# Kernel tuning notes

Measured on AMD Instinct MI355X. Metric: run time of the kernel, lower is better.

The kernel has to match this reference:

```python
import jax, jax.numpy as jnp
import numpy as np

B, N, M, DIM, H, DH = 2, 2048, 2048, 512, 8, 64
INNER = H * DH
SCALE = DH ** -0.5  # cosine_sim=False default
EPS = 1e-5


def layer_norm(x, g, b):
    mu = x.mean(-1, keepdims=True)
    var = ((x - mu) ** 2).mean(-1, keepdims=True)
    return (x - mu) * jax.lax.rsqrt(var + EPS) * g + b


def setup_inputs() -> dict:
    key = jax.random.key(0)
    ks = jax.random.split(key, 8)
    x = jax.random.normal(ks[0], (B, N, DIM), dtype=jnp.float32)
    context = jax.random.normal(ks[1], (B, M, DIM), dtype=jnp.float32)
    mask = jax.random.randint(ks[2], (B, M), 0, 2).astype(bool)
    Wq = jax.random.normal(ks[3], (DIM, INNER), dtype=jnp.float32) * 0.02
    Wkv = jax.random.normal(ks[4], (DIM, 2 * INNER), dtype=jnp.float32) * 0.02
    Wo = jax.random.normal(ks[5], (INNER, DIM), dtype=jnp.float32) * 0.02
    ln_g = jnp.ones((DIM,), jnp.float32)
    ln_b = jnp.zeros((DIM,), jnp.float32)
    lno_g = jnp.ones((DIM,), jnp.float32)
    lno_b = jnp.zeros((DIM,), jnp.float32)
    return {"x": x, "context": context, "mask": mask, "ln_g": ln_g, "ln_b": ln_b,
            "Wq": Wq, "Wkv": Wkv, "Wo": Wo, "lno_g": lno_g, "lno_b": lno_b}


def reference(x, context, mask, ln_g, ln_b, Wq, Wkv, Wo, lno_g, lno_b):
    b, n, _ = x.shape
    xn = layer_norm(x, ln_g, ln_b)
    ctx = context  # norm_context=False -> Identity
    q = (xn @ Wq).reshape(b, n, H, DH).transpose(0, 2, 1, 3)          # b h n d
    kv = ctx @ Wkv
    k, v = jnp.split(kv, 2, axis=-1)
    k = k.reshape(b, -1, H, DH).transpose(0, 2, 1, 3)                 # b h m d
    v = v.reshape(b, -1, H, DH).transpose(0, 2, 1, 3)
    q = q * SCALE
    k = k * SCALE
    sim = jnp.einsum('bhid,bhjd->bhij', q, k)                         # b h n m (256 MB)
    max_neg = -jnp.finfo(sim.dtype).max
    sim = jnp.where(mask[:, None, None, :], sim, max_neg)
    attn = jax.nn.softmax(sim.astype(jnp.float32), axis=-1).astype(sim.dtype)
    out = jnp.einsum('bhij,bhjd->bhid', attn, v)
    out = out.transpose(0, 2, 1, 3).reshape(b, n, INNER)
    return layer_norm(out @ Wo, lno_g, lno_b)
```

## Files before the change

kernel.cpp:

```cpp
#include <hip/hip_runtime.h>
#include <stdint.h>

typedef float f32x4 __attribute__((ext_vector_type(4)));
typedef float f32x16 __attribute__((ext_vector_type(16)));
typedef __bf16 bf16x8 __attribute__((ext_vector_type(8)));
typedef unsigned int uint2v __attribute__((ext_vector_type(2)));

#define MFMA16(a,b,c) __builtin_amdgcn_mfma_f32_16x16x32_bf16((a),(b),(c),0,0,0)
#define MFMA32(a,b,c) __builtin_amdgcn_mfma_f32_32x32x16_bf16((a),(b),(c),0,0,0)

__device__ __forceinline__ unsigned short f2bf(float f){
  unsigned int u = __float_as_uint(f);
  u += 0x7FFFu + ((u >> 16) & 1u);
  return (unsigned short)(u >> 16);
}

__device__ __forceinline__ unsigned cvtpk(float lo, float hi){
  unsigned r;
  asm volatile("v_cvt_pk_bf16_f32 %0, %1, %2" : "=v"(r) : "v"(lo), "v"(hi));
  return r;
}

__device__ __forceinline__ float fexp2(float x){
#if __has_builtin(__builtin_amdgcn_exp2f)
  return __builtin_amdgcn_exp2f(x);
#else
  return exp2f(x);
#endif
}

__device__ __forceinline__ void plswap(unsigned &a, unsigned &b){
#if __has_builtin(__builtin_amdgcn_permlane32_swap)
  uint2v r = __builtin_amdgcn_permlane32_swap(a, b, false, false);
  a = r[0]; b = r[1];
#else
  unsigned xa = __shfl_xor(a, 32), xb = __shfl_xor(b, 32);
  int hi = (threadIdx.x & 63) >> 5;
  unsigned na = hi ? xb : a;
  unsigned nb = hi ? b : xa;
  a = na; b = nb;
#endif
}

__device__ __forceinline__ void stage16(const unsigned short* g, unsigned short* l){
  __builtin_amdgcn_global_load_lds(
      (const __attribute__((address_space(1))) void*)g,
      (__attribute__((address_space(3))) void*)l, 16, 0, 0);
}

__global__ __launch_bounds__(256) void k_prep(
    const float* __restrict__ Wq, const float* __restrict__ Wkv, const float* __restrict__ Wo,
    const float* __restrict__ x, const float* __restrict__ ln_g, const float* __restrict__ ln_b,
    const float* __restrict__ ctx, const int* __restrict__ mask,
    unsigned short* __restrict__ WqT, unsigned short* __restrict__ WkvT, unsigned short* __restrict__ WoT,
    unsigned short* __restrict__ xn, unsigned short* __restrict__ cb, unsigned int* __restrict__ mb)
{
  __shared__ float tile[32][33];
  const int bid = blockIdx.x, t = threadIdx.x;
  if (bid < 1024) {
    const float* W; unsigned short* WT; int N, bx, by;
    if (bid < 256)      { W = Wq;  WT = WqT;  N = 512;  bx = bid & 15;        by = bid >> 4; }
    else if (bid < 768) { W = Wkv; WT = WkvT; N = 1024; bx = (bid-256) & 31;  by = (bid-256) >> 5; }
    else                { W = Wo;  WT = WoT;  N = 512;  bx = (bid-768) & 15;  by = (bid-768) >> 4; }
    const int tx = t & 31, ty = t >> 5;
    #pragma unroll
    for (int i = 0; i < 4; i++)
      tile[ty + i*8][tx] = W[(size_t)(by*32 + ty + i*8) * N + bx*32 + tx];
    __syncthreads();
    #pragma unroll
    for (int i = 0; i < 4; i++)
      WT[(size_t)(bx*32 + ty + i*8) * 512 + by*32 + tx] = f2bf(tile[tx][ty + i*8]);
  } else if (bid < 2048) {
    int row = (bid - 1024) * 4 + (t >> 6);
    int lane = t & 63;
    const float4* xr = (const float4*)(x + (size_t)row * 512);
    float4 a = xr[lane], c = xr[64 + lane];
    float s = a.x + a.y + a.z + a.w + c.x + c.y + c.z + c.w;
    #pragma unroll
    for (int o = 32; o; o >>= 1) s += __shfl_xor(s, o);
    float mu = s * (1.0f / 512.0f);
    float va = (a.x-mu)*(a.x-mu) + (a.y-mu)*(a.y-mu) + (a.z-mu)*(a.z-mu) + (a.w-mu)*(a.w-mu)
             + (c.x-mu)*(c.x-mu) + (c.y-mu)*(c.y-mu) + (c.z-mu)*(c.z-mu) + (c.w-mu)*(c.w-mu);
    #pragma unroll
    for (int o = 32; o; o >>= 1) va += __shfl_xor(va, o);
    float inv = rsqrtf(va * (1.0f / 512.0f) + 1e-5f);
    const float4* gp = (const float4*)ln_g;
    const float4* bp = (const float4*)ln_b;
    float4 g0 = gp[lane], g1 = gp[64 + lane], b0 = bp[lane], b1 = bp[64 + lane];
    ushort4* op = (ushort4*)(xn + (size_t)row * 512);
    op[lane]      = make_ushort4(f2bf((a.x-mu)*inv*g0.x + b0.x), f2bf((a.y-mu)*inv*g0.y + b0.y),
                                 f2bf((a.z-mu)*inv*g0.z + b0.z), f2bf((a.w-mu)*inv*g0.w + b0.w));
    op[64 + lane] = make_ushort4(f2bf((c.x-mu)*inv*g1.x + b1.x), f2bf((c.y-mu)*inv*g1.y + b1.y),
                                 f2bf((c.z-mu)*inv*g1.z + b1.z), f2bf((c.w-mu)*inv*g1.w + b1.w));
  } else if (bid < 4096) {
    int i = (bid - 2048) * 256 + t;
    float4 v = ((const float4*)ctx)[i];
    ((ushort4*)cb)[i] = make_ushort4(f2bf(v.x), f2bf(v.y), f2bf(v.z), f2bf(v.w));
  } else {
    int g = (bid - 4096) * 4 + (t >> 6);
    int ln = t & 63;
    int v = mask[g * 64 + ln];
    unsigned long long bb = __ballot(v != 0);
    if (ln == 0) { mb[g*2] = (unsigned)bb; mb[g*2+1] = (unsigned)(bb >> 32); }
  }
}

__global__ __launch_bounds__(256) void k_layernorm_f(
    const float* __restrict__ X, const float* __restrict__ G,
    const float* __restrict__ Bt, float* __restrict__ out)
{
  int row = blockIdx.x * 4 + (threadIdx.x >> 6);
  int lane = threadIdx.x & 63;
  const float4* xr = (const float4*)(X + (size_t)row * 512);
  float4 a = xr[lane], c = xr[64 + lane];
  float s = a.x + a.y + a.z + a.w + c.x + c.y + c.z + c.w;
  #pragma unroll
  for (int o = 32; o; o >>= 1) s += __shfl_xor(s, o);
  float mu = s * (1.0f / 512.0f);
  float va = (a.x-mu)*(a.x-mu) + (a.y-mu)*(a.y-mu) + (a.z-mu)*(a.z-mu) + (a.w-mu)*(a.w-mu)
           + (c.x-mu)*(c.x-mu) + (c.y-mu)*(c.y-mu) + (c.z-mu)*(c.z-mu) + (c.w-mu)*(c.w-mu);
  #pragma unroll
  for (int o = 32; o; o >>= 1) va += __shfl_xor(va, o);
  float inv = rsqrtf(va * (1.0f / 512.0f) + 1e-5f);
  const float4* gp = (const float4*)G;
  const float4* bp = (const float4*)Bt;
  float4 g0 = gp[lane], g1 = gp[64 + lane], b0 = bp[lane], b1 = bp[64 + lane];
  float4 y0, y1;
  y0.x = (a.x-mu)*inv*g0.x + b0.x; y0.y = (a.y-mu)*inv*g0.y + b0.y;
  y0.z = (a.z-mu)*inv*g0.z + b0.z; y0.w = (a.w-mu)*inv*g0.w + b0.w;
  y1.x = (c.x-mu)*inv*g1.x + b1.x; y1.y = (c.y-mu)*inv*g1.y + b1.y;
  y1.z = (c.z-mu)*inv*g1.z + b1.z; y1.w = (c.w-mu)*inv*g1.w + b1.w;
  float4* op = (float4*)(out + (size_t)row * 512);
  op[lane] = y0; op[64 + lane] = y1;
}

template<int MODE>
__device__ __forceinline__ void gemm_body(
    const unsigned short* __restrict__ A, const unsigned short* __restrict__ BT,
    void* __restrict__ out0, void* __restrict__ out1, int bx, int by,
    unsigned short* smem)
{
  unsigned short* As = smem;
  unsigned short* Bs = smem + 2*64*64;
  const int t = threadIdx.x;
  const int lane = t & 63, l16 = lane & 15, lhi = lane >> 4;
  const int w = t >> 6, wm = w >> 1, wn = w & 1;
  const int rowBase = by * 64;
  const int colBase = bx * 128;
  const int srr = lane >> 3, scw = lane & 7;

  f32x4 acc[2][4];
  #pragma unroll
  for (int i = 0; i < 2; i++)
    #pragma unroll
    for (int j = 0; j < 4; j++)
      acc[i][j] = f32x4{0.f, 0.f, 0.f, 0.f};

  auto STAGE = [&](int buf, int kt) {
    unsigned short* Ab = As + buf * 4096;
    unsigned short* Bb = Bs + buf * 8192;
    #pragma unroll
    for (int i = 0; i < 2; i++) {
      int rr = i * 32 + w * 8 + srr;
      stage16(A + (size_t)(rowBase + rr) * 512 + kt * 64 + ((scw ^ (rr & 7)) * 8),
              Ab + (i * 32 + w * 8) * 64);
    }
    #pragma unroll
    for (int i = 0; i < 4; i++) {
      int rr = i * 32 + w * 8 + srr;
      stage16(BT + (size_t)(colBase + rr) * 512 + kt * 64 + ((scw ^ (rr & 7)) * 8),
              Bb + (i * 32 + w * 8) * 64);
    }
  };

  STAGE(0, 0);
  __syncthreads();
  for (int kt = 0; kt < 8; ++kt) {
    const int buf = kt & 1;
    if (kt < 7) STAGE(buf ^ 1, kt + 1);
    const char* Ab = (const char*)(As + buf * 4096);
    const char* Bb = (const char*)(Bs + buf * 8192);
    #pragma unroll
    for (int ks = 0; ks < 2; ++ks) {
      bf16x8 af[2], bb[4];
      #pragma unroll
      for (int mi = 0; mi < 2; mi++) {
        int rr = wm * 32 + mi * 16 + l16;
        int cc = ks * 4 + lhi;
        af[mi] = *(const bf16x8*)(Ab + rr * 128 + ((cc ^ (rr & 7)) * 16));
      }
      #pragma unroll
      for (int ni = 0; ni < 4; ni++) {
        int rr = wn * 64 + ni * 16 + l16;
        int cc = ks * 4 + lhi;
        bb[ni] = *(const bf16x8*)(Bb + rr * 128 + ((cc ^ (rr & 7)) * 16));
      }
      #pragma unroll
      for (int mi = 0; mi < 2; mi++)
        #pragma unroll
        for (int ni = 0; ni < 4; ni++)
          acc[mi][ni] = MFMA16(af[mi], bb[ni], acc[mi][ni]);
    }
    __syncthreads();
  }

  if constexpr (MODE == 2) {
    const int r0 = rowBase + wm * 32 + lhi * 4;
    const int c0 = colBase + wn * 64 + l16;
    #pragma unroll
    for (int mi = 0; mi < 2; mi++)
      #pragma unroll
      for (int ni = 0; ni < 4; ni++)
        #pragma unroll
        for (int r = 0; r < 4; r++)
          ((float*)out0)[(size_t)(r0 + mi * 16 + r) * 512 + c0 + ni * 16] = acc[mi][ni][r];
  } else {
    unsigned short* stg = smem;
    const bool isV = (MODE == 1) && (colBase >= 512);
    if (!isV) {
      #pragma unroll
      for (int mi = 0; mi < 2; mi++) {
        int rl = wm * 32 + mi * 16 + lhi * 4;
        int tl = rl >> 5;
        #pragma unroll
        for (int ni = 0; ni < 4; ni++) {
          int cl = wn * 64 + ni * 16 + l16;
          int hl = cl >> 6, d = cl & 63;
          int rbase = (hl * 2 + tl) * 2048 + (d >> 4) * 512 + 256 * ((d >> 3) & 1) + (d & 7);
          #pragma unroll
          for (int r = 0; r < 4; r++)
            stg[rbase + ((rl + r) & 31) * 8] = f2bf(acc[mi][ni][r]);
        }
      }
    } else {
      #pragma unroll
      for (int mi = 0; mi < 2; mi++) {
        int rl = wm * 32 + mi * 16 + lhi * 4;
        int tl = rl >> 5, kvr = rl & 31;
        #pragma unroll
        for (int ni = 0; ni < 4; ni++) {
          int cl = wn * 64 + ni * 16 + l16;
          int hl = cl >> 6, d = cl & 63;
          int off = (hl * 2 + tl) * 2048 + (d >> 5) * 1024 + ((kvr >> 4) & 1) * 512
                  + ((d & 31) + 32 * ((kvr >> 3) & 1)) * 8 + (kvr & 7);
          ushort4 p = make_ushort4(f2bf(acc[mi][ni][0]), f2bf(acc[mi][ni][1]),
                                   f2bf(acc[mi][ni][2]), f2bf(acc[mi][ni][3]));
          *(ushort4*)(stg + off) = p;
        }
      }
    }
    __syncthreads();
    const int bb2 = rowBase >> 11;
    const int hh0 = (colBase & 511) >> 6;
    const int tile0 = (rowBase & 2047) >> 5;
    unsigned short* gout = (unsigned short*)(isV ? out1 : out0);
    #pragma unroll
    for (int ridx = 0; ridx < 4; ridx++) {
      int hl = ridx >> 1, tl = ridx & 1;
      size_t gb = ((size_t)((bb2 * 8 + hh0 + hl) * 64 + tile0 + tl)) * 2048 + t * 8;
      *(uint4*)(gout + gb) = *(const uint4*)(stg + ridx * 2048 + t * 8);
    }
  }
}

__global__ __launch_bounds__(256, 2) void k_qkv(
    const unsigned short* __restrict__ xn, const unsigned short* __restrict__ WqT,
    unsigned short* __restrict__ Qp,
    const unsigned short* __restrict__ cb, const unsigned short* __restrict__ WkvT,
    unsigned short* __restrict__ Kp, unsigned short* __restrict__ Vp)
{
  __shared__ __align__(16) unsigned short smem[2*64*64 + 2*128*64];
  const int bid = blockIdx.x;
  const int xcd = bid & 7, loc = bid >> 3;
  const int mloc = loc / 12, ct = loc % 12;
  const int mtile = xcd * 8 + mloc;
  if (ct < 4) gemm_body<0>(xn, WqT, Qp, nullptr, ct, mtile, smem);
  else        gemm_body<1>(cb, WkvT, Kp, Vp, ct - 4, mtile, smem);
}

__global__ __launch_bounds__(256, 2) void k_oproj(
    const unsigned short* __restrict__ ao, const unsigned short* __restrict__ WoT,
    float* __restrict__ proj)
{
  __shared__ __align__(16) unsigned short smem[2*64*64 + 2*128*64];
  const int bid = blockIdx.x;
  const int xcd = bid & 7, loc = bid >> 3;
  const int mloc = loc >> 2, ct = loc & 3;
  const int mtile = xcd * 8 + mloc;
  gemm_body<2>(ao, WoT, proj, nullptr, ct, mtile, smem);
}

__global__ __launch_bounds__(256, 3) void k_attn(
    const unsigned short* __restrict__ Qp, const unsigned short* __restrict__ Kp,
    const unsigned short* __restrict__ Vp, const unsigned int* __restrict__ mb,
    unsigned short* __restrict__ O)
{
  __shared__ __align__(16) float mbuf[3][64][34];
  const int t = threadIdx.x, lane = t & 63, q5 = lane & 31, hi = lane >> 5;
  const int w = t >> 6;
  const int bid = blockIdx.x;
  const int bh = (bid & 7) * 2 + (bid >> 9);
  const int qt = (bid >> 3) & 63;
  const int q0 = qt * 32;
  const int b = bh >> 3, h = bh & 7;
  const float C2f = 0.022542110013890053f;

  bf16x8 qf[4];
  {
    const unsigned short* qp = Qp + (size_t)(bh * 64 + qt) * 2048 + lane * 8;
    #pragma unroll
    for (int kk = 0; kk < 4; kk++) qf[kk] = *(const bf16x8*)(qp + kk * 512);
  }
  const unsigned short* kpb = Kp + (size_t)bh * 131072 + lane * 8;
  const unsigned short* vpb = Vp + (size_t)bh * 131072 + lane * 8;
  const unsigned int* mbp = mb + b * 64;

  float mrun = -3e38f, lrun = 0.f;
  f32x16 acc0, acc1;
  #pragma unroll
  for (int i = 0; i < 16; i++) { acc0[i] = 0.f; acc1[i] = 0.f; }

  bf16x8 kf[4], vf[4];
  auto loadK = [&](int tile) {
    #pragma unroll
    for (int kk = 0; kk < 4; kk++)
      kf[kk] = *(const bf16x8*)(kpb + (size_t)tile * 2048 + kk * 512);
  };
  auto loadV = [&](int tile) {
    #pragma unroll
    for (int i = 0; i < 4; i++)
      vf[i] = *(const bf16x8*)(vpb + (size_t)tile * 2048 + i * 512);
  };

  const int tb = w * 16;
  loadK(tb); loadV(tb);
  for (int it = 0; it < 16; ++it) {
    const int ti = tb + it;

    f32x16 s;
    #pragma unroll
    for (int i = 0; i < 16; i++) s[i] = 0.f;
    #pragma unroll
    for (int kk = 0; kk < 4; kk++) s = MFMA32(kf[kk], qf[kk], s);
    if (it < 15) loadK(ti + 1);

    float m0 = fmaxf(fmaxf(s[0], s[1]),  fmaxf(s[2], s[3]));
    float m1 = fmaxf(fmaxf(s[4], s[5]),  fmaxf(s[6], s[7]));
    float m2 = fmaxf(fmaxf(s[8], s[9]),  fmaxf(s[10], s[11]));
    float m3 = fmaxf(fmaxf(s[12], s[13]), fmaxf(s[14], s[15]));
    float tmax = fmaxf(fmaxf(m0, m1), fmaxf(m2, m3));
    tmax = fmaxf(tmax, __shfl_xor(tmax, 32));
    if (!__all(tmax <= mrun + 400.f)) {
      float mnew = fmaxf(mrun, tmax);
      float sf = fexp2((mrun - mnew) * C2f);
      lrun *= sf;
      #pragma unroll
      for (int i = 0; i < 16; i++) { acc0[i] *= sf; acc1[i] *= sf; }
      mrun = mnew;
    }
    unsigned mh = mbp[ti] >> (hi * 4);
    float nb = -mrun * C2f;
    float p[16];
    #pragma unroll
    for (int r = 0; r < 16; r++) {
      float pv = fexp2(fmaf(s[r], C2f, nb));
      p[r] = ((mh >> ((r & 3) + 8 * (r >> 2))) & 1u) ? pv : 0.f;
    }
    float rsa = (p[0] + p[1]) + (p[2] + p[3]);
    float rsb = (p[4] + p[5]) + (p[6] + p[7]);
    float rsc = (p[8] + p[9]) + (p[10] + p[11]);
    float rsd = (p[12] + p[13]) + (p[14] + p[15]);
    float rs = (rsa + rsb) + (rsc + rsd);
    rs += __shfl_xor(rs, 32);
    lrun += rs;

    unsigned wd[8];
    #pragma unroll
    for (int i = 0; i < 8; i++) wd[i] = cvtpk(p[2 * i], p[2 * i + 1]);
    plswap(wd[0], wd[2]); plswap(wd[1], wd[3]);
    plswap(wd[4], wd[6]); plswap(wd[5], wd[7]);
    union { unsigned u[4]; bf16x8 v; } U0, U1;
    U0.u[0] = wd[0]; U0.u[1] = wd[1]; U0.u[2] = wd[2]; U0.u[3] = wd[3];
    U1.u[0] = wd[4]; U1.u[1] = wd[5]; U1.u[2] = wd[6]; U1.u[3] = wd[7];

    acc0 = MFMA32(vf[0], U0.v, acc0);
    acc0 = MFMA32(vf[1], U1.v, acc0);
    acc1 = MFMA32(vf[2], U0.v, acc1);
    acc1 = MFMA32(vf[3], U1.v, acc1);
    if (it < 15) loadV(ti + 1);
  }

  if (w) {
    #pragma unroll
    for (int i = 0; i < 16; i++) { mbuf[w-1][lane][i] = acc0[i]; mbuf[w-1][lane][16 + i] = acc1[i]; }
    mbuf[w-1][lane][32] = mrun; mbuf[w-1][lane][33] = lrun;
  }
  __syncthreads();
  if (!w) {
    float mo[3], lo[3];
    #pragma unroll
    for (int wv = 0; wv < 3; wv++) { mo[wv] = mbuf[wv][lane][32]; lo[wv] = mbuf[wv][lane][33]; }
    float mN = fmaxf(fmaxf(mrun, mo[0]), fmaxf(mo[1], mo[2]));
    float sf0 = fexp2((mrun - mN) * C2f);
    float sfv[3];
    float lsum = lrun * sf0;
    #pragma unroll
    for (int wv = 0; wv < 3; wv++) { sfv[wv] = fexp2((mo[wv] - mN) * C2f); lsum += lo[wv] * sfv[wv]; }
    float linv = 1.f / lsum;
    float a2[32];
    #pragma unroll
    for (int i = 0; i < 16; i++) {
      float v0 = acc0[i] * sf0, v1 = acc1[i] * sf0;
      #pragma unroll
      for (int wv = 0; wv < 3; wv++) {
        v0 += mbuf[wv][lane][i] * sfv[wv];
        v1 += mbuf[wv][lane][16 + i] * sfv[wv];
      }
      a2[i] = v0 * linv;
      a2[16 + i] = v1 * linv;
    }
    unsigned short* ot = (unsigned short*)&mbuf[0][0][0];
    #pragma unroll
    for (int d2 = 0; d2 < 2; d2++)
      #pragma unroll
      for (int i = 0; i < 8; i++) {
        int d0 = ((2 * i) & 3) + 8 * (i >> 1) + 4 * hi + 32 * d2;
        unsigned wv2 = cvtpk(a2[d2 * 16 + 2 * i], a2[d2 * 16 + 2 * i + 1]);
        *(unsigned*)(ot + q5 * 72 + d0) = wv2;
      }
    #pragma unroll
    for (int it2 = 0; it2 < 4; ++it2) {
      int row = (lane >> 3) + it2 * 8, ch = lane & 7;
      uint4 val = *(const uint4*)(ot + row * 72 + ch * 8);
      *(uint4*)(O + ((size_t)(b * 2048 + q0 + row)) * 512 + h * 64 + ch * 8) = val;
    }
  }
}

extern "C" void kernel_launch(void* const* d_in, const int* in_sizes, int n_in,
                              void* d_out, int out_size, void* d_ws, size_t ws_size,
                              hipStream_t stream) {
  const float* x     = (const float*)d_in[0];
  const float* ctx   = (const float*)d_in[1];
  const int*   mask  = (const int*)d_in[2];
  const float* ln_g  = (const float*)d_in[3];
  const float* ln_b  = (const float*)d_in[4];
  const float* Wq    = (const float*)d_in[5];
  const float* Wkv   = (const float*)d_in[6];
  const float* Wo    = (const float*)d_in[7];
  const float* lno_g = (const float*)d_in[8];
  const float* lno_b = (const float*)d_in[9];
  float* out = (float*)d_out;

  char* ws = (char*)d_ws;
  unsigned short* WqT  = (unsigned short*)(ws + 0);
  unsigned short* WkvT = (unsigned short*)(ws + (size_t)1 * (1 << 19));
  unsigned short* WoT  = (unsigned short*)(ws + (size_t)3 * (1 << 19));
  unsigned short* xn   = (unsigned short*)(ws + (size_t)2  * (1 << 20));
  unsigned short* cb   = (unsigned short*)(ws + (size_t)6  * (1 << 20));
  unsigned short* Qp   = (unsigned short*)(ws + (size_t)10 * (1 << 20));
  unsigned short* Kp   = (unsigned short*)(ws + (size_t)14 * (1 << 20));
  unsigned short* Vp   = (unsigned short*)(ws + (size_t)18 * (1 << 20));
  unsigned short* ao   = (unsigned short*)(ws + (size_t)22 * (1 << 20));
  float* proj          = (float*)(ws + (size_t)26 * (1 << 20));
  unsigned int* mbw    = (unsigned int*)(ws + (size_t)26 * (1 << 20));

  k_prep<<<4112, 256, 0, stream>>>(Wq, Wkv, Wo, x, ln_g, ln_b, ctx, mask,
                                   WqT, WkvT, WoT, xn, cb, mbw);
  k_qkv<<<768, 256, 0, stream>>>(xn, WqT, Qp, cb, WkvT, Kp, Vp);
  k_attn<<<1024, 256, 0, stream>>>(Qp, Kp, Vp, mbw, ao);
  k_oproj<<<256, 256, 0, stream>>>(ao, WoT, proj);
  k_layernorm_f<<<1024, 256, 0, stream>>>(proj, lno_g, lno_b, out);
}
```

Measured before the change: 63.13 us.

## Give each attention wave its own query tile over all keys, dropping split-K merge

Measured after the change: 78.68 us. 1.25x slower.

```diff
diff --git a/kernel.cpp b/kernel.cpp
--- a/kernel.cpp
+++ b/kernel.cpp
@@ -290,17 +290,17 @@
   gemm_body<2>(ao, WoT, proj, nullptr, ct, mtile, smem);
 }
 
-__global__ __launch_bounds__(256, 3) void k_attn(
+__global__ __launch_bounds__(256, 2) void k_attn(
     const unsigned short* __restrict__ Qp, const unsigned short* __restrict__ Kp,
     const unsigned short* __restrict__ Vp, const unsigned int* __restrict__ mb,
     unsigned short* __restrict__ O)
 {
-  __shared__ __align__(16) float mbuf[3][64][34];
+  __shared__ __align__(16) unsigned short otbuf[4][32 * 72];
   const int t = threadIdx.x, lane = t & 63, q5 = lane & 31, hi = lane >> 5;
   const int w = t >> 6;
   const int bid = blockIdx.x;
-  const int bh = (bid & 7) * 2 + (bid >> 9);
-  const int qt = (bid >> 3) & 63;
+  const int bh = (bid & 7) * 2 + ((bid >> 7) & 1);
+  const int qt = ((bid >> 3) & 15) * 4 + w;
   const int q0 = qt * 32;
   const int b = bh >> 3, h = bh & 7;
   const float C2f = 0.022542110013890053f;
@@ -332,17 +332,14 @@
       vf[i] = *(const bf16x8*)(vpb + (size_t)tile * 2048 + i * 512);
   };
 
-  const int tb = w * 16;
-  loadK(tb); loadV(tb);
-  for (int it = 0; it < 16; ++it) {
-    const int ti = tb + it;
-
+  loadK(0); loadV(0);
+  for (int it = 0; it < 64; ++it) {
     f32x16 s;
     #pragma unroll
     for (int i = 0; i < 16; i++) s[i] = 0.f;
     #pragma unroll
     for (int kk = 0; kk < 4; kk++) s = MFMA32(kf[kk], qf[kk], s);
-    if (it < 15) loadK(ti + 1);
+    if (it < 63) loadK(it + 1);
 
     float m0 = fmaxf(fmaxf(s[0], s[1]),  fmaxf(s[2], s[3]));
     float m1 = fmaxf(fmaxf(s[4], s[5]),  fmaxf(s[6], s[7]));
@@ -358,7 +355,7 @@
       for (int i = 0; i < 16; i++) { acc0[i] *= sf; acc1[i] *= sf; }
       mrun = mnew;
     }
-    unsigned mh = mbp[ti] >> (hi * 4);
+    unsigned mh = mbp[it] >> (hi * 4);
     float nb = -mrun * C2f;
     float p[16];
     #pragma unroll
@@ -387,46 +384,20 @@
     acc0 = MFMA32(vf[1], U1.v, acc0);
     acc1 = MFMA32(vf[2], U0.v, acc1);
     acc1 = MFMA32(vf[3], U1.v, acc1);
-    if (it < 15) loadV(ti + 1);
-  }
-
-  if (w) {
-    #pragma unroll
-    for (int i = 0; i < 16; i++) { mbuf[w-1][lane][i] = acc0[i]; mbuf[w-1][lane][16 + i] = acc1[i]; }
-    mbuf[w-1][lane][32] = mrun; mbuf[w-1][lane][33] = lrun;
-  }
-  __syncthreads();
-  if (!w) {
-    float mo[3], lo[3];
-    #pragma unroll
-    for (int wv = 0; wv < 3; wv++) { mo[wv] = mbuf[wv][lane][32]; lo[wv] = mbuf[wv][lane][33]; }
-    float mN = fmaxf(fmaxf(mrun, mo[0]), fmaxf(mo[1], mo[2]));
-    float sf0 = fexp2((mrun - mN) * C2f);
-    float sfv[3];
-    float lsum = lrun * sf0;
-    #pragma unroll
-    for (int wv = 0; wv < 3; wv++) { sfv[wv] = fexp2((mo[wv] - mN) * C2f); lsum += lo[wv] * sfv[wv]; }
-    float linv = 1.f / lsum;
-    float a2[32];
-    #pragma unroll
-    for (int i = 0; i < 16; i++) {
-      float v0 = acc0[i] * sf0, v1 = acc1[i] * sf0;
-      #pragma unroll
-      for (int wv = 0; wv < 3; wv++) {
-        v0 += mbuf[wv][lane][i] * sfv[wv];
-        v1 += mbuf[wv][lane][16 + i] * sfv[wv];
-      }
-      a2[i] = v0 * linv;
-      a2[16 + i] = v1 * linv;
-    }
-    unsigned short* ot = (unsigned short*)&mbuf[0][0][0];
+    if (it < 63) loadV(it + 1);
+  }
+
+  {
+    float linv = 1.f / lrun;
+    unsigned short* ot = otbuf[w];
     #pragma unroll
     for (int d2 = 0; d2 < 2; d2++)
       #pragma unroll
       for (int i = 0; i < 8; i++) {
         int d0 = ((2 * i) & 3) + 8 * (i >> 1) + 4 * hi + 32 * d2;
-        unsigned wv2 = cvtpk(a2[d2 * 16 + 2 * i], a2[d2 * 16 + 2 * i + 1]);
-        *(unsigned*)(ot + q5 * 72 + d0) = wv2;
+        float lo = (d2 ? acc1[2 * i]     : acc0[2 * i])     * linv;
+        float hv = (d2 ? acc1[2 * i + 1] : acc0[2 * i + 1]) * linv;
+        *(unsigned*)(ot + q5 * 72 + d0) = cvtpk(lo, hv);
       }
     #pragma unroll
     for (int it2 = 0; it2 < 4; ++it2) {
@@ -468,7 +439,7 @@
   k_prep<<<4112, 256, 0, stream>>>(Wq, Wkv, Wo, x, ln_g, ln_b, ctx, mask,
                                    WqT, WkvT, WoT, xn, cb, mbw);
   k_qkv<<<768, 256, 0, stream>>>(xn, WqT, Qp, cb, WkvT, Kp, Vp);
-  k_attn<<<1024, 256, 0, stream>>>(Qp, Kp, Vp, mbw, ao);
+  k_attn<<<256, 256, 0, stream>>>(Qp, Kp, Vp, mbw, ao);
   k_oproj<<<256, 256, 0, stream>>>(ao, WoT, proj);
   k_layernorm_f<<<1024, 256, 0, stream>>>(proj, lno_g, lno_b, out);
 }
```
